# Optimization experiments

Hardware: AMD Instinct MI355X
Metric: run time of the kernel (lower is better)

Reference implementation:

```python
import jax, jax.numpy as jnp
import numpy as np

B, N, DIM = 2, 2048, 1024
H, DH = 16, 64
INNER = H * DH  # 1024
SCALE = DH ** -0.5
EPS = 1e-5


def setup_inputs() -> dict:
    key = jax.random.key(0)
    ks = jax.random.split(key, 7)
    s = 0.02
    return {
        "x": jax.random.normal(ks[0], (B, N, DIM), dtype=jnp.float32),
        "ln_gamma": jnp.ones((DIM,), jnp.float32),
        "ln_beta": jnp.zeros((DIM,), jnp.float32),
        "W_qkv": jax.random.normal(ks[1], (DIM, 3 * INNER), jnp.float32) * s,
        "b_qkv": jnp.zeros((3 * INNER,), jnp.float32),
        "W_out": jax.random.normal(ks[2], (INNER, DIM), jnp.float32) * s,
        "b_out": jnp.zeros((DIM,), jnp.float32),
    }


def reference(x, ln_gamma, ln_beta, W_qkv, b_qkv, W_out, b_out):
    # LayerNorm over last dim
    mu = jnp.mean(x, axis=-1, keepdims=True)
    var = jnp.mean(jnp.square(x - mu), axis=-1, keepdims=True)
    xn = (x - mu) * jax.lax.rsqrt(var + EPS) * ln_gamma + ln_beta
    # QKV projection
    qkv = xn @ W_qkv + b_qkv                      # [b, n, 3*inner]
    q, k, v = jnp.split(qkv, 3, axis=-1)
    # [b, n, (h d)] -> [b, h, n, d]
    to_heads = lambda t: t.reshape(B, N, H, DH).transpose(0, 2, 1, 3)
    q, k, v = to_heads(q), to_heads(k), to_heads(v)
    # naive attention (explicit score matrix, matching the original)
    qk = jnp.einsum('bhnd,bhmd->bhnm', q, k) * SCALE
    attn = jax.nn.softmax(qk, axis=-1)
    out = jnp.einsum('bhnm,bhmd->bhnd', attn, v)  # [b, h, n, d]
    out = out.transpose(0, 2, 1, 3).reshape(B, N, INNER)
    return out @ W_out + b_out
```

## Files before the change

### kernel.cpp

```cpp
#include <hip/hip_runtime.h>

typedef unsigned short u16;
typedef unsigned int   u32;
typedef __attribute__((ext_vector_type(4)))  float  f32x4;
typedef __attribute__((ext_vector_type(8)))  short  s16x8;

__device__ __forceinline__ u16 f2bf(float f) {
  unsigned u = __builtin_bit_cast(unsigned, f);
  u += 0x7FFFu + ((u >> 16) & 1u);
  return (u16)(u >> 16);
}

__device__ __forceinline__ float exp2g(float x) { return __builtin_amdgcn_exp2f(x); }

__device__ __forceinline__ void gload16(const void* g, void* l) {
  __builtin_amdgcn_global_load_lds(
      (const __attribute__((address_space(1))) void*)g,
      (__attribute__((address_space(3))) void*)l, 16, 0, 0);
}

__global__ __launch_bounds__(256) void ln_kernel(
    const float* __restrict__ x, const float* __restrict__ gamma,
    const float* __restrict__ beta, u16* __restrict__ xn)
{
  const int row = blockIdx.x, tid = threadIdx.x;
  const float* xr = x + (size_t)row * 1024;
  float4 v = *(const float4*)(xr + tid * 4);
  float s  = v.x + v.y + v.z + v.w;
  float s2 = v.x*v.x + v.y*v.y + v.z*v.z + v.w*v.w;
#pragma unroll
  for (int off = 32; off >= 1; off >>= 1) {
    s  += __shfl_xor(s,  off);
    s2 += __shfl_xor(s2, off);
  }
  __shared__ float red[8];
  const int w = tid >> 6, l = tid & 63;
  if (l == 0) { red[w] = s; red[w + 4] = s2; }
  __syncthreads();
  s  = red[0] + red[1] + red[2] + red[3];
  s2 = red[4] + red[5] + red[6] + red[7];
  const float mu  = s * (1.0f / 1024.0f);
  const float var = s2 * (1.0f / 1024.0f) - mu * mu;
  const float rs  = rsqrtf(var + 1e-5f);
  float4 g  = *(const float4*)(gamma + tid * 4);
  float4 be = *(const float4*)(beta  + tid * 4);
  ushort4 o;
  o.x = f2bf((v.x - mu) * rs * g.x + be.x);
  o.y = f2bf((v.y - mu) * rs * g.y + be.y);
  o.z = f2bf((v.z - mu) * rs * g.z + be.z);
  o.w = f2bf((v.w - mu) * rs * g.w + be.w);
  *(ushort4*)(xn + (size_t)row * 1024 + tid * 4) = o;
}

__global__ void transpose_cvt(const float* __restrict__ in, u16* __restrict__ out,
                              int R, int C)
{
  __shared__ float t[32][33];
  const int bc = blockIdx.x * 32, br = blockIdx.y * 32;
  const int x = threadIdx.x;
#pragma unroll
  for (int i = threadIdx.y; i < 32; i += 8)
    t[i][x] = in[(size_t)(br + i) * C + bc + x];
  __syncthreads();
#pragma unroll
  for (int i = threadIdx.y; i < 32; i += 8)
    out[(size_t)(bc + i) * R + br + x] = f2bf(t[x][i]);
}

__device__ __forceinline__ void store_out(float* p, float v) { *p = v; }
__device__ __forceinline__ void store_out(u16* p, float v)   { *p = f2bf(v); }

template <typename OutT>
__global__ __launch_bounds__(256) void gemm_bt(
    const u16* __restrict__ A, const u16* __restrict__ Bt,
    const float* __restrict__ bias, OutT* __restrict__ C,
    int M, int N, int K)
{
  __shared__ u16 As[2][128 * 32];
  __shared__ u16 Bs[2][128 * 32];
  const int tid = threadIdx.x;
  const int w = tid >> 6, l = tid & 63;
  const int g = l >> 4, li = l & 15;
  const int bm = blockIdx.y * 128, bn = blockIdx.x * 128;
  const int wr = (w >> 1) * 64, wc = (w & 1) * 64;

  f32x4 acc[4][4] = {};

  const int ar0 = tid >> 2,          as0 = tid & 3;
  const int ar1 = (tid + 256) >> 2,  as1 = (tid + 256) & 3;
  const u16* pa0 = A  + (size_t)(bm + ar0) * K + 8 * (as0 ^ (ar0 & 3));
  const u16* pa1 = A  + (size_t)(bm + ar1) * K + 8 * (as1 ^ (ar1 & 3));
  const u16* pb0 = Bt + (size_t)(bn + ar0) * K + 8 * (as0 ^ (ar0 & 3));
  const u16* pb1 = Bt + (size_t)(bn + ar1) * K + 8 * (as1 ^ (ar1 & 3));

  auto stage = [&](int b, int kt) {
    gload16(pa0 + kt, &As[b][w * 512]);
    gload16(pa1 + kt, &As[b][2048 + w * 512]);
    gload16(pb0 + kt, &Bs[b][w * 512]);
    gload16(pb1 + kt, &Bs[b][2048 + w * 512]);
  };

  stage(0, 0);

  int buf = 0;
  for (int kt = 0; kt < K; kt += 32) {
    __syncthreads();
    if (kt + 32 < K) stage(buf ^ 1, kt + 32);

    const u16* as = &As[buf][0];
    const u16* bs = &Bs[buf][0];

    s16x8 af[4], bf[4];
#pragma unroll
    for (int m = 0; m < 4; ++m) {
      const int row = wr + m * 16 + li;
      af[m] = *(const s16x8*)(as + row * 32 + 8 * (g ^ (row & 3)));
    }
#pragma unroll
    for (int n = 0; n < 4; ++n) {
      const int row = wc + n * 16 + li;
      bf[n] = *(const s16x8*)(bs + row * 32 + 8 * (g ^ (row & 3)));
    }
    __builtin_amdgcn_s_setprio(1);
#pragma unroll
    for (int m = 0; m < 4; ++m)
#pragma unroll
      for (int n = 0; n < 4; ++n)
        acc[m][n] = __builtin_amdgcn_mfma_f32_16x16x32_bf16(af[m], bf[n], acc[m][n], 0, 0, 0);
    __builtin_amdgcn_s_setprio(0);

    buf ^= 1;
  }

#pragma unroll
  for (int n = 0; n < 4; ++n) {
    const int col = bn + wc + n * 16 + li;
    const float bv = bias[col];
#pragma unroll
    for (int m = 0; m < 4; ++m) {
      const int row0 = bm + wr + m * 16 + g * 4;
#pragma unroll
      for (int r = 0; r < 4; ++r)
        store_out(C + (size_t)(row0 + r) * N + col, acc[m][n][r] + bv);
    }
  }
}

__global__ __launch_bounds__(256, 4) void attn_kernel(
    const u16* __restrict__ qkv, u16* __restrict__ outp)
{
  __shared__ u16 Ks[2][4096];
  __shared__ u16 Vt[4096];
  __shared__ u16 Pl[4 * 1024];

  const int tid = threadIdx.x;
  const int w = tid >> 6, l = tid & 63;
  const int g = l >> 4, li = l & 15;

  const int lb = (blockIdx.x & 7) * 128 + (blockIdx.x >> 3);
  const int qt = lb & 31;
  const int h  = (lb >> 5) & 15;
  const int bb = lb >> 9;
  const size_t baserow = (size_t)bb * 2048;

  const int qbase = qt * 64 + w * 16;
  const u16* qp = qkv + (baserow + qbase + li) * 3072 + h * 64 + 8 * g;
  const s16x8 qf0 = *(const s16x8*)(qp);
  const s16x8 qf1 = *(const s16x8*)(qp + 32);

  const int kr0 = tid >> 3,         kc0 = tid & 7;
  const int kr1 = (tid + 256) >> 3, kc1 = (tid + 256) & 7;
  const u16* kg0 = qkv + (baserow + kr0) * 3072 + 1024 + h * 64 + 8 * (kc0 ^ (kr0 & 7));
  const u16* kg1 = qkv + (baserow + kr1) * 3072 + 1024 + h * 64 + 8 * (kc1 ^ (kr1 & 7));

  const int vp = tid >> 3, dg = tid & 7;
  const u16* vgA = qkv + (baserow + 2 * vp)     * 3072 + 2048 + h * 64 + 8 * dg;
  const u16* vgB = qkv + (baserow + 2 * vp + 1) * 3072 + 2048 + h * 64 + 8 * dg;

  auto issueK = [&](int b, int t) {
    const size_t koff = (size_t)t * (64 * 3072);
    gload16(kg0 + koff, &Ks[b][w * 512]);
    gload16(kg1 + koff, &Ks[b][2048 + w * 512]);
  };

  const float C1  = 0.18033688f;
  const float THR = 11.5416f;
  float M[4];
#pragma unroll
  for (int r = 0; r < 4; ++r) M[r] = -1e30f;
  f32x4 o[4] = {}, os = {};

  s16x8 ones;
#pragma unroll
  for (int j = 0; j < 8; ++j) ones[j] = (short)0x3F80;

  char* Pw = (char*)(Pl + w * 1024);

  issueK(0, 0);
  s16x8 va = *(const s16x8*)vgA;
  s16x8 vb = *(const s16x8*)vgB;

  int buf = 0;
  for (int t = 0; t < 32; ++t) {
#pragma unroll
    for (int j = 0; j < 8; ++j) {
      const int d = 8 * dg + j;
      const u32 val = (u32)(u16)va[j] | ((u32)(u16)vb[j] << 16);
      *(u32*)((char*)Vt + d * 128 + ((4 * vp) ^ ((((d ^ (d >> 3)) & 7)) << 4))) = val;
    }
    __syncthreads();

    if (t < 31) {
      issueK(buf ^ 1, t + 1);
      const size_t koff = (size_t)(t + 1) * (64 * 3072);
      va = *(const s16x8*)(vgA + koff);
      vb = *(const s16x8*)(vgB + koff);
    }

    const u16* kb = &Ks[buf][0];

    f32x4 s[4] = {};
    __builtin_amdgcn_s_setprio(1);
#pragma unroll
    for (int nk = 0; nk < 4; ++nk) {
      const int kvr = nk * 16 + li;
      const s16x8 kf0 = *(const s16x8*)((const char*)kb + kvr * 128 + 16 * ((0 + g) ^ (kvr & 7)));
      const s16x8 kf1 = *(const s16x8*)((const char*)kb + kvr * 128 + 16 * ((4 + g) ^ (kvr & 7)));
      s[nk] = __builtin_amdgcn_mfma_f32_16x16x32_bf16(qf0, kf0, s[nk], 0, 0, 0);
      s[nk] = __builtin_amdgcn_mfma_f32_16x16x32_bf16(qf1, kf1, s[nk], 0, 0, 0);
    }
    __builtin_amdgcn_s_setprio(0);

    float lm[4];
    bool need = false;
#pragma unroll
    for (int r = 0; r < 4; ++r) {
      lm[r] = fmaxf(fmaxf(s[0][r], s[1][r]), fmaxf(s[2][r], s[3][r])) * C1;
      need |= (lm[r] > M[r] + THR);
    }
    if (__any(need)) {
#pragma unroll
      for (int r = 0; r < 4; ++r) {
        float mx = lm[r];
#pragma unroll
        for (int off = 1; off < 16; off <<= 1) mx = fmaxf(mx, __shfl_xor(mx, off));
        const float mn = fmaxf(M[r], mx);
        const float a = exp2g(M[r] - mn);
        M[r] = mn;
        os[r] *= a;
#pragma unroll
        for (int nd = 0; nd < 4; ++nd) o[nd][r] *= a;
      }
    }

#pragma unroll
    for (int r = 0; r < 4; ++r)
#pragma unroll
      for (int nk = 0; nk < 4; ++nk)
        s[nk][r] = exp2g(fmaf(s[nk][r], C1, -M[r]));

#pragma unroll
    for (int nk = 0; nk < 4; ++nk)
#pragma unroll
      for (int r = 0; r < 4; ++r) {
        const int q = g * 4 + r;
        *(u16*)(Pw + q * 128 + ((nk * 32 + li * 2) ^ (g << 5))) = f2bf(s[nk][r]);
      }
    asm volatile("s_waitcnt lgkmcnt(0)" ::: "memory");

    __builtin_amdgcn_s_setprio(1);
#pragma unroll
    for (int ks = 0; ks < 2; ++ks) {
      const s16x8 pf = *(const s16x8*)(Pw + li * 128 + ((ks * 64 + 16 * g) ^ (((li >> 2) & 3) << 5)));
#pragma unroll
      for (int nd = 0; nd < 4; ++nd) {
        const int d = nd * 16 + li;
        const s16x8 vf = *(const s16x8*)((char*)Vt + d * 128 + ((ks * 64 + 16 * g) ^ (((d ^ (d >> 3)) & 7) << 4)));
        o[nd] = __builtin_amdgcn_mfma_f32_16x16x32_bf16(pf, vf, o[nd], 0, 0, 0);
      }
      os = __builtin_amdgcn_mfma_f32_16x16x32_bf16(pf, ones, os, 0, 0, 0);
    }
    __builtin_amdgcn_s_setprio(0);

    __syncthreads();
    buf ^= 1;
  }

#pragma unroll
  for (int r = 0; r < 4; ++r) {
    const float inv = 1.0f / os[r];
    const size_t row = baserow + qbase + g * 4 + r;
#pragma unroll
    for (int nd = 0; nd < 4; ++nd)
      outp[row * 1024 + h * 64 + nd * 16 + li] = f2bf(o[nd][r] * inv);
  }
}

extern "C" void kernel_launch(void* const* d_in, const int* in_sizes, int n_in,
                              void* d_out, int out_size, void* d_ws, size_t ws_size,
                              hipStream_t stream)
{
  const float* x     = (const float*)d_in[0];
  const float* gamma = (const float*)d_in[1];
  const float* beta  = (const float*)d_in[2];
  const float* Wqkv  = (const float*)d_in[3];
  const float* bqkv  = (const float*)d_in[4];
  const float* Wout  = (const float*)d_in[5];
  const float* bout  = (const float*)d_in[6];
  float* out = (float*)d_out;

  char* ws = (char*)d_ws;
  u16* xn     = (u16*)(ws);
  u16* wqkv_t = (u16*)(ws + ((size_t)8  << 20));
  u16* wout_t = (u16*)(ws + ((size_t)14 << 20));
  u16* qkv    = (u16*)(ws + ((size_t)16 << 20));
  u16* attn   = (u16*)(ws + ((size_t)40 << 20));

  ln_kernel<<<4096, 256, 0, stream>>>(x, gamma, beta, xn);
  transpose_cvt<<<dim3(96, 32), dim3(32, 8), 0, stream>>>(Wqkv, wqkv_t, 1024, 3072);
  transpose_cvt<<<dim3(32, 32), dim3(32, 8), 0, stream>>>(Wout, wout_t, 1024, 1024);
  gemm_bt<u16><<<dim3(24, 32), 256, 0, stream>>>(xn, wqkv_t, bqkv, qkv, 4096, 3072, 1024);
  attn_kernel<<<1024, 256, 0, stream>>>(qkv, attn);
  gemm_bt<float><<<dim3(8, 32), 256, 0, stream>>>(attn, wout_t, bout, out, 4096, 1024, 1024);
}
```

Measured before the change: 143.6 us.

## Transpose MFMA operands so each lane owns one query row in attention

Swaps the A/B operands of the QK^T and PV MFMAs so the accumulator holds scores transposed, giving each lane a single query row. The per-row max becomes a lane-local reduction plus two cross-lane shuffles, and the running max, rescale and normalizer collapse from four values to one. P is packed with v_cvt_pk_bf16_f32 and written as 8-byte LDS stores instead of scalar u16 stores, and the output is written as ushort4 vector stores. This cuts shuffle, VALU and LDS store instruction counts in the softmax path, but the result depends on the new P swizzle and operand layout being correct.

```diff
diff --git a/kernel.cpp b/kernel.cpp
--- a/kernel.cpp
+++ b/kernel.cpp
@@ -2,6 +2,7 @@
 
 typedef unsigned short u16;
 typedef unsigned int   u32;
+typedef __attribute__((ext_vector_type(2)))  unsigned u32x2;
 typedef __attribute__((ext_vector_type(4)))  float  f32x4;
 typedef __attribute__((ext_vector_type(8)))  short  s16x8;
 
@@ -185,9 +186,7 @@
 
   const float C1  = 0.18033688f;
   const float THR = 11.5416f;
-  float M[4];
-#pragma unroll
-  for (int r = 0; r < 4; ++r) M[r] = -1e30f;
+  float M = -1e30f;
   f32x4 o[4] = {}, os = {};
 
   s16x8 ones;
@@ -195,6 +194,7 @@
   for (int j = 0; j < 8; ++j) ones[j] = (short)0x3F80;
 
   char* Pw = (char*)(Pl + w * 1024);
+  const int pswz = (li & 7) << 4;
 
   issueK(0, 0);
   s16x8 va = *(const s16x8*)vgA;
@@ -226,59 +226,56 @@
       const int kvr = nk * 16 + li;
       const s16x8 kf0 = *(const s16x8*)((const char*)kb + kvr * 128 + 16 * ((0 + g) ^ (kvr & 7)));
       const s16x8 kf1 = *(const s16x8*)((const char*)kb + kvr * 128 + 16 * ((4 + g) ^ (kvr & 7)));
-      s[nk] = __builtin_amdgcn_mfma_f32_16x16x32_bf16(qf0, kf0, s[nk], 0, 0, 0);
-      s[nk] = __builtin_amdgcn_mfma_f32_16x16x32_bf16(qf1, kf1, s[nk], 0, 0, 0);
+      s[nk] = __builtin_amdgcn_mfma_f32_16x16x32_bf16(kf0, qf0, s[nk], 0, 0, 0);
+      s[nk] = __builtin_amdgcn_mfma_f32_16x16x32_bf16(kf1, qf1, s[nk], 0, 0, 0);
     }
     __builtin_amdgcn_s_setprio(0);
 
-    float lm[4];
-    bool need = false;
-#pragma unroll
-    for (int r = 0; r < 4; ++r) {
-      lm[r] = fmaxf(fmaxf(s[0][r], s[1][r]), fmaxf(s[2][r], s[3][r])) * C1;
-      need |= (lm[r] > M[r] + THR);
-    }
-    if (__any(need)) {
-#pragma unroll
-      for (int r = 0; r < 4; ++r) {
-        float mx = lm[r];
-#pragma unroll
-        for (int off = 1; off < 16; off <<= 1) mx = fmaxf(mx, __shfl_xor(mx, off));
-        const float mn = fmaxf(M[r], mx);
-        const float a = exp2g(M[r] - mn);
-        M[r] = mn;
-        os[r] *= a;
-#pragma unroll
-        for (int nd = 0; nd < 4; ++nd) o[nd][r] *= a;
-      }
-    }
-
-#pragma unroll
-    for (int r = 0; r < 4; ++r)
-#pragma unroll
-      for (int nk = 0; nk < 4; ++nk)
-        s[nk][r] = exp2g(fmaf(s[nk][r], C1, -M[r]));
+    float lm = fmaxf(fmaxf(s[0][0], s[0][1]), fmaxf(s[0][2], s[0][3]));
+#pragma unroll
+    for (int nk = 1; nk < 4; ++nk)
+      lm = fmaxf(lm, fmaxf(fmaxf(s[nk][0], s[nk][1]), fmaxf(s[nk][2], s[nk][3])));
+    lm = fmaxf(lm, __shfl_xor(lm, 16));
+    lm = fmaxf(lm, __shfl_xor(lm, 32));
+    lm *= C1;
+
+    if (__any(lm > M + THR)) {
+      const float mn = fmaxf(M, lm);
+      const float a = exp2g(M - mn);
+      M = mn;
+      os[0] *= a;
+#pragma unroll
+      for (int nd = 0; nd < 4; ++nd)
+#pragma unroll
+        for (int r = 0; r < 4; ++r) o[nd][r] *= a;
+    }
 
 #pragma unroll
     for (int nk = 0; nk < 4; ++nk)
 #pragma unroll
-      for (int r = 0; r < 4; ++r) {
-        const int q = g * 4 + r;
-        *(u16*)(Pw + q * 128 + ((nk * 32 + li * 2) ^ (g << 5))) = f2bf(s[nk][r]);
-      }
+      for (int r = 0; r < 4; ++r)
+        s[nk][r] = exp2g(fmaf(s[nk][r], C1, -M));
+
+#pragma unroll
+    for (int nk = 0; nk < 4; ++nk) {
+      u32 lo, hi;
+      asm("v_cvt_pk_bf16_f32 %0, %1, %2" : "=v"(lo) : "v"(s[nk][0]), "v"(s[nk][1]));
+      asm("v_cvt_pk_bf16_f32 %0, %1, %2" : "=v"(hi) : "v"(s[nk][2]), "v"(s[nk][3]));
+      *(u32x2*)(Pw + li * 128 + ((nk * 32 + 8 * g) ^ pswz)) = (u32x2){lo, hi};
+    }
     asm volatile("s_waitcnt lgkmcnt(0)" ::: "memory");
 
     __builtin_amdgcn_s_setprio(1);
 #pragma unroll
     for (int ks = 0; ks < 2; ++ks) {
-      const s16x8 pf = *(const s16x8*)(Pw + li * 128 + ((ks * 64 + 16 * g) ^ (((li >> 2) & 3) << 5)));
+      const s16x8 pf = *(const s16x8*)(Pw + li * 128 + ((ks * 64 + 16 * g) ^ pswz));
 #pragma unroll
       for (int nd = 0; nd < 4; ++nd) {
         const int d = nd * 16 + li;
         const s16x8 vf = *(const s16x8*)((char*)Vt + d * 128 + ((ks * 64 + 16 * g) ^ (((d ^ (d >> 3)) & 7) << 4)));
-        o[nd] = __builtin_amdgcn_mfma_f32_16x16x32_bf16(pf, vf, o[nd], 0, 0, 0);
+        o[nd] = __builtin_amdgcn_mfma_f32_16x16x32_bf16(vf, pf, o[nd], 0, 0, 0);
       }
-      os = __builtin_amdgcn_mfma_f32_16x16x32_bf16(pf, ones, os, 0, 0, 0);
+      os = __builtin_amdgcn_mfma_f32_16x16x32_bf16(ones, pf, os, 0, 0, 0);
     }
     __builtin_amdgcn_s_setprio(0);
 
@@ -286,13 +283,16 @@
     buf ^= 1;
   }
 
-#pragma unroll
-  for (int r = 0; r < 4; ++r) {
-    const float inv = 1.0f / os[r];
-    const size_t row = baserow + qbase + g * 4 + r;
-#pragma unroll
-    for (int nd = 0; nd < 4; ++nd)
-      outp[row * 1024 + h * 64 + nd * 16 + li] = f2bf(o[nd][r] * inv);
+  const float inv = 1.0f / os[0];
+  const size_t row = baserow + qbase + li;
+#pragma unroll
+  for (int nd = 0; nd < 4; ++nd) {
+    ushort4 st;
+    st.x = f2bf(o[nd][0] * inv);
+    st.y = f2bf(o[nd][1] * inv);
+    st.z = f2bf(o[nd][2] * inv);
+    st.w = f2bf(o[nd][3] * inv);
+    *(ushort4*)(outp + row * 1024 + h * 64 + nd * 16 + 4 * g) = st;
   }
 }
 
```

Result: faster. 135.7 us (-5.5%).
